# Optimization experiments

Hardware: AMD Instinct MI355X
Metric: run time of the kernel (lower is better)

## Reference

```python
import jax, jax.numpy as jnp
import numpy as np

# irreps: input = 32x0e + 16x1o (dim 80); key/query/value = 8x0e + 4x1o (dim 20); lmax = 1
N_NODES = 10000
N_EDGES = 160000
MUL0_IN, MUL1_IN = 32, 16
MUL0_OUT, MUL1_OUT = 8, 4
NUM_BASIS = 32
HIDDEN = 32
MAX_RADIUS = 2.5
NUM_NEIGHBORS = 32
# per-edge fully-connected TP weight blocks (paths: 0e*0e->0e, 1o*1o->0e, 0e*1o->1o, 1o*0e->1o)
S00 = MUL0_IN * MUL0_OUT    # 256
S110 = MUL1_IN * MUL0_OUT   # 128
S01 = MUL0_IN * MUL1_OUT    # 128
S10 = MUL1_IN * MUL1_OUT    # 64
WNUMEL = S00 + S110 + S01 + S10  # 576
SQRT3 = 1.7320508075688772


def _split_irreps(z, mul0, mul1):
    return z[:, :mul0], z[:, mul0:].reshape(-1, mul1, 3)


def _basis_net(rb, w1, w2):
    # e3nn FullyConnectedNet([num_basis, 32, weight_numel], silu): x @ W / sqrt(fan_in)
    h = jax.nn.silu(rb @ w1 / jnp.sqrt(float(NUM_BASIS)))
    return h @ w2 / jnp.sqrt(float(HIDDEN))


def _edge_tp(x0, x1, Y1, w):
    # FullyConnectedTensorProduct with per-edge weights w [E, WNUMEL].
    # e3nn component/element normalization: path_weight = sqrt(dim(ir_out)/fan_in),
    # fan_in per output irrep = MUL0_IN + MUL1_IN = 48; CG(1,1,0)=CG(0,1,1)=delta/sqrt(3).
    c = 1.0 / jnp.sqrt(float(MUL0_IN + MUL1_IN))
    w00 = w[:, :S00].reshape(-1, MUL0_IN, MUL0_OUT)
    w110 = w[:, S00:S00 + S110].reshape(-1, MUL1_IN, MUL0_OUT)
    w01 = w[:, S00 + S110:S00 + S110 + S01].reshape(-1, MUL0_IN, MUL1_OUT)
    w10 = w[:, S00 + S110 + S01:].reshape(-1, MUL1_IN, MUL1_OUT)
    x1dotY = jnp.einsum('eum,em->eu', x1, Y1)  # [E, MUL1_IN]
    out0 = c * (jnp.einsum('euw,eu->ew', w00, x0)
                + jnp.einsum('euw,eu->ew', w110, x1dotY) / SQRT3)
    out1 = c * (jnp.einsum('euw,eu->ew', w01, x0)[:, :, None] * Y1[:, None, :]
                + jnp.einsum('euw,eum->ewm', w10, x1))
    return out0, out1  # [E, MUL0_OUT], [E, MUL1_OUT, 3]


def _forward(x, pos, w_q0, w_q1, w_kb1, w_kb2, w_vb1, w_vb2, w_sim0, w_sim1, edge_index):
    src, dst = edge_index[0], edge_index[1]
    vec = pos[src] - pos[dst]                                   # [E,3]
    r = jnp.sqrt(jnp.sum(vec * vec, axis=1) + 1e-24)            # [E]
    # bessel soft_one_hot_linspace (cutoff=True), scaled by sqrt(num_basis)
    n = jnp.arange(1, NUM_BASIS + 1, dtype=jnp.float32)
    rb = jnp.sqrt(2.0 / MAX_RADIUS) * jnp.sin(n * jnp.pi * r[:, None] / MAX_RADIUS) / r[:, None]
    rb = rb * jnp.sqrt(float(NUM_BASIS))
    # soft_unit_step(10*(1 - r/max_radius)) = exp(-1/t) for t > 0 else 0
    t = 10.0 * (1.0 - r / MAX_RADIUS)
    cutoff = jnp.where(t > 0.0, jnp.exp(-1.0 / jnp.maximum(t, 1e-12)), 0.0)
    # spherical harmonics lmax=1, 'component' norm: Y0 = 1, Y1 = sqrt(3)*unit_vec
    Y1 = SQRT3 * vec / r[:, None]
    x0, x1 = _split_irreps(x, MUL0_IN, MUL1_IN)
    # o3.Linear query projection: independent per-l blocks, / sqrt(fan_in)
    q0 = x0 @ w_q0 / jnp.sqrt(float(MUL0_IN))                   # [N,8]
    q1 = jnp.einsum('num,uw->nwm', x1, w_q1) / jnp.sqrt(float(MUL1_IN))  # [N,4,3]
    wk = _basis_net(rb, w_kb1, w_kb2)                           # [E,576]
    wv = _basis_net(rb, w_vb1, w_vb2)                           # [E,576]
    x0s, x1s = x0[src], x1[src]
    k0, k1 = _edge_tp(x0s, x1s, Y1, wk)
    v0, v1 = _edge_tp(x0s, x1s, Y1, wv)
    # similarity TP (query x key -> 0e): fan_in = 8*8 + 4*4 = 80
    cs = 1.0 / jnp.sqrt(float(MUL0_OUT ** 2 + MUL1_OUT ** 2))
    sim = cs * (jnp.einsum('uv,eu,ev->e', w_sim0, q0[src], k0)
                + jnp.einsum('uv,eum,evm->e', w_sim1, q1[src], k1) / SQRT3)
    logits = cutoff * sim
    # segment softmax grouped by src node
    m = jax.ops.segment_max(logits, src, num_segments=N_NODES)
    m = jnp.where(jnp.isfinite(m), m, 0.0)
    ex = jnp.exp(logits - m[src])
    den = jax.ops.segment_sum(ex, src, num_segments=N_NODES)
    attn = ex / den[src]                                        # [E]
    a = jnp.sqrt(jax.nn.relu(attn))[:, None]                    # [E,1]
    vals = jnp.concatenate([v0, v1.reshape(-1, MUL1_OUT * 3)], axis=1)  # [E,20]
    return jax.ops.segment_sum(a * vals, dst, num_segments=N_NODES) / NUM_NEIGHBORS


def setup_inputs():
    key = jax.random.key(0)
    ks = jax.random.split(key, 11)
    return {
        'x': jax.random.normal(ks[0], (N_NODES, MUL0_IN + 3 * MUL1_IN), jnp.float32),
        'pos': jax.random.uniform(ks[1], (N_NODES, 3), jnp.float32) * MAX_RADIUS,
        'w_q0': jax.random.normal(ks[2], (MUL0_IN, MUL0_OUT), jnp.float32),
        'w_q1': jax.random.normal(ks[3], (MUL1_IN, MUL1_OUT), jnp.float32),
        'w_kb1': jax.random.normal(ks[4], (NUM_BASIS, HIDDEN), jnp.float32),
        'w_kb2': jax.random.normal(ks[5], (HIDDEN, WNUMEL), jnp.float32),
        'w_vb1': jax.random.normal(ks[6], (NUM_BASIS, HIDDEN), jnp.float32),
        'w_vb2': jax.random.normal(ks[7], (HIDDEN, WNUMEL), jnp.float32),
        'w_sim0': jax.random.normal(ks[8], (MUL0_OUT, MUL0_OUT), jnp.float32),
        'w_sim1': jax.random.normal(ks[9], (MUL1_OUT, MUL1_OUT), jnp.float32),
        'edge_index': jax.random.randint(ks[10], (2, N_EDGES), 0, N_NODES, dtype=jnp.int32),
    }


def reference(x, pos, w_q0, w_q1, w_kb1, w_kb2, w_vb1, w_vb2, w_sim0, w_sim1, edge_index):
    return _forward(x, pos, w_q0, w_q1, w_kb1, w_kb2, w_vb1, w_vb2, w_sim0, w_sim1, edge_index)
```

## Files before the change

kernel.cpp:

```cpp
#include <hip/hip_runtime.h>
#include <hip/hip_fp16.h>
#include <math.h>

#define NN 10000
#define NE 160000

typedef _Float16 half8 __attribute__((ext_vector_type(8)));
typedef __attribute__((ext_vector_type(4))) float f32x4;

constexpr float SQRT3f    = 1.7320508075688772f;
constexpr float ISQRT3    = 0.57735026918962576f;
constexpr float ISQRT32   = 0.17677669529663687f;
constexpr float C_TP      = 0.14433756729740645f;
constexpr float CSIM      = 0.11180339887498949f;
constexpr float PREB      = 5.0596442562694074f;
constexpr float PI_OVER_R = 1.2566370614359172f;
constexpr float INV_RMAX  = 0.4f;
constexpr float HKSC      = C_TP * ISQRT32;
constexpr float DEN_SCALE = 16777216.0f;
constexpr float DEN_INV   = 1.0f / 16777216.0f;
constexpr float OUT_SCALE = 8388608.0f;
constexpr float OUT_INV   = 1.0f / 8388608.0f;

__device__ __forceinline__ unsigned fkey(float f) {
  unsigned u = __float_as_uint(f);
  return (u & 0x80000000u) ? ~u : (u | 0x80000000u);
}
__device__ __forceinline__ float funkey(unsigned k) {
  return (k & 0x80000000u) ? __uint_as_float(k ^ 0x80000000u)
                           : __uint_as_float(~k);
}
__device__ __forceinline__ unsigned short f2h(float f) {
  return __half_as_ushort(__float2half(f));
}

__device__ __forceinline__ int origcol(int n) {
  if (n >= 576) return 512 + (n - 576);
  int w = n / 48, u = n % 48;
  if (w < 8) return (u < 32) ? (u * 8 + w) : (256 + (u - 32) * 8 + w);
  return (u < 32) ? (384 + u * 4 + (w - 8)) : -1;
}

__global__ void __launch_bounds__(256) k_prep(
    const float* __restrict__ w_vb1, const float* __restrict__ w_vb2,
    const float* __restrict__ w_kb1,
    float* __restrict__ W1vt, float* __restrict__ W1kt,
    unsigned short* __restrict__ Wtv)
{
  int tid = blockIdx.x * 256 + threadIdx.x;
  if (tid < 640 * 32) {
    int n = tid >> 5, h = tid & 31;
    int oc = origcol(n);
    float v = (oc >= 0) ? w_vb2[h * 576 + oc] : 0.0f;
    Wtv[n * 32 + h] = f2h(v);
  }
  if (tid < 1024) {
    int h = tid >> 5, n2 = tid & 31;
    W1vt[h * 32 + n2] = w_vb1[n2 * 32 + h];
  } else if (tid < 2048) {
    int j = tid - 1024;
    int h = j >> 5, n2 = j & 31;
    W1kt[h * 32 + n2] = w_kb1[n2 * 32 + h];
  }
}

__global__ void __launch_bounds__(256) k_node(
    const float* __restrict__ x, const float* __restrict__ w_q0,
    const float* __restrict__ w_q1, const float* __restrict__ w_sim0,
    const float* __restrict__ w_sim1,
    float* __restrict__ qs0, float* __restrict__ qs1)
{
  int n = blockIdx.x * 256 + threadIdx.x;
  if (n >= NN) return;
  float x0[32], x1f[48];
  const float4* xr = (const float4*)(x + 80 * n);
#pragma unroll
  for (int i = 0; i < 8; ++i) {
    float4 v = xr[i];
    x0[4*i]=v.x; x0[4*i+1]=v.y; x0[4*i+2]=v.z; x0[4*i+3]=v.w;
  }
#pragma unroll
  for (int i = 0; i < 12; ++i) {
    float4 v = xr[8 + i];
    x1f[4*i]=v.x; x1f[4*i+1]=v.y; x1f[4*i+2]=v.z; x1f[4*i+3]=v.w;
  }
  float q0[8];
#pragma unroll
  for (int w = 0; w < 8; ++w) {
    float a = 0.f;
#pragma unroll
    for (int u = 0; u < 32; ++u) a = fmaf(x0[u], w_q0[u * 8 + w], a);
    q0[w] = a * ISQRT32;
  }
  float q1[12];
#pragma unroll
  for (int w = 0; w < 4; ++w)
#pragma unroll
    for (int m = 0; m < 3; ++m) {
      float a = 0.f;
#pragma unroll
      for (int u = 0; u < 16; ++u) a = fmaf(x1f[3*u+m], w_q1[u*4+w], a);
      q1[w * 3 + m] = a * 0.25f;
    }
#pragma unroll
  for (int v = 0; v < 8; ++v) {
    float a = 0.f;
#pragma unroll
    for (int u = 0; u < 8; ++u) a = fmaf(w_sim0[u * 8 + v], q0[u], a);
    qs0[n * 8 + v] = CSIM * a;
  }
#pragma unroll
  for (int v = 0; v < 4; ++v)
#pragma unroll
    for (int m = 0; m < 3; ++m) {
      float a = 0.f;
#pragma unroll
      for (int u = 0; u < 4; ++u) a = fmaf(w_sim1[u*4+v], q1[u*3+m], a);
      qs1[n * 12 + v * 3 + m] = (CSIM * ISQRT3) * a;
    }
}

template <int HALF>
__global__ void __launch_bounds__(256) k_nodeF(
    const float* __restrict__ x, const float* __restrict__ w_kb2,
    const float* __restrict__ qs0g, const float* __restrict__ qs1g,
    float* __restrict__ nodeF)
{
  __shared__ float W2f[16 * 577];
  __shared__ float ndl[16][100];

  const int tid = threadIdx.x;
  const int nb = blockIdx.x * 16;

#pragma unroll
  for (int i = 0; i < 36; ++i) {
    int idx = i * 256 + tid;
    int row = idx / 576, col = idx - row * 576;
    W2f[row * 577 + col] = w_kb2[(HALF * 16 + row) * 576 + col];
  }
  for (int j = tid; j < 1600; j += 256) {
    int nn = j / 100, jj = j - nn * 100;
    int n = nb + nn;
    float v;
    if (jj < 80)      v = x[80 * n + jj];
    else if (jj < 88) v = qs0g[8 * n + (jj - 80)];
    else              v = qs1g[12 * n + (jj - 88)];
    ndl[nn][jj] = v;
  }
  __syncthreads();

  const int nn = tid >> 4, hh = tid & 15;
  const float* Wh = W2f + hh * 577;
  const float* nd = ndl[nn];

  float t14 = 0.f;
#pragma unroll
  for (int a = 0; a < 32; ++a) {
    float tmp = 0.f;
#pragma unroll
    for (int v = 0; v < 8; ++v) tmp = fmaf(Wh[a * 8 + v], nd[80 + v], tmp);
    t14 = fmaf(tmp, nd[a], t14);
  }
#pragma unroll
  for (int a = 0; a < 16; ++a)
#pragma unroll
    for (int v = 0; v < 4; ++v) {
      float dotv = fmaf(nd[32 + 3*a], nd[88 + 3*v],
                   fmaf(nd[32 + 3*a + 1], nd[88 + 3*v + 1],
                        nd[32 + 3*a + 2] * nd[88 + 3*v + 2]));
      t14 = fmaf(Wh[512 + a * 4 + v], dotv, t14);
    }

  float F0 = 0.f, F1 = 0.f, F2 = 0.f;
#pragma unroll
  for (int a = 0; a < 16; ++a) {
    float q = 0.f;
#pragma unroll
    for (int v = 0; v < 8; ++v) q = fmaf(Wh[256 + a * 8 + v], nd[80 + v], q);
    F0 = fmaf(q, nd[32 + 3*a],     F0);
    F1 = fmaf(q, nd[32 + 3*a + 1], F1);
    F2 = fmaf(q, nd[32 + 3*a + 2], F2);
  }
  F0 *= ISQRT3; F1 *= ISQRT3; F2 *= ISQRT3;
#pragma unroll
  for (int v = 0; v < 4; ++v) {
    float rr = 0.f;
#pragma unroll
    for (int a = 0; a < 32; ++a) rr = fmaf(Wh[384 + a * 4 + v], nd[a], rr);
    F0 = fmaf(rr, nd[88 + 3*v],     F0);
    F1 = fmaf(rr, nd[88 + 3*v + 1], F1);
    F2 = fmaf(rr, nd[88 + 3*v + 2], F2);
  }

  const int n = nb + nn, h = HALF * 16 + hh;
  *(float4*)(nodeF + (size_t)(n * 32 + h) * 4) = make_float4(t14, F0, F1, F2);
}

__global__ void __launch_bounds__(256) k_edgelogit(
    const float* __restrict__ pos,
    const int* __restrict__ esrc, const int* __restrict__ edst,
    const float* __restrict__ W1vt, const float* __restrict__ W1kt,
    const float* __restrict__ nodeF,
    unsigned* __restrict__ hv2, float* __restrict__ geom,
    float* __restrict__ logits, unsigned* __restrict__ mkey)
{
  int e = blockIdx.x * 256 + threadIdx.x;
  if (e >= NE) return;
  int s = esrc[e], d = edst[e];
  float vx = pos[3*s]   - pos[3*d];
  float vy = pos[3*s+1] - pos[3*d+1];
  float vz = pos[3*s+2] - pos[3*d+2];
  float r = sqrtf(fmaf(vx, vx, fmaf(vy, vy, vz * vz)) + 1e-24f);
  float inv_r = 1.0f / r;

  float rb[32];
  {
    float sn, cth;
    sincosf(PI_OVER_R * r, &sn, &cth);
    float twoc = 2.0f * cth, pre = PREB * inv_r, snm1 = 0.0f;
#pragma unroll
    for (int n = 0; n < 32; ++n) {
      rb[n] = pre * sn;
      float t = fmaf(twoc, sn, -snm1);
      snm1 = sn; sn = t;
    }
  }
  float Yx = SQRT3f * vx * inv_r, Yy = SQRT3f * vy * inv_r, Yz = SQRT3f * vz * inv_r;
  float tc = 10.0f * (1.0f - r * INV_RMAX);
  float cut = (tc > 0.0f) ? __expf(-1.0f / tc) : 0.0f;
  *(float4*)(geom + 4 * e) = make_float4(Yx, Yy, Yz, cut);

  const float4* nf = (const float4*)(nodeF) + (size_t)s * 32;
  float sim = 0.f;
#pragma unroll 1
  for (int h2 = 0; h2 < 16; ++h2) {
    const float* wv0 = W1vt + (2 * h2) * 32;
    const float* wv1 = wv0 + 32;
    const float* wk0 = W1kt + (2 * h2) * 32;
    const float* wk1 = wk0 + 32;
    float av0 = 0.f, av1 = 0.f, ak0 = 0.f, ak1 = 0.f;
#pragma unroll
    for (int n = 0; n < 32; ++n) {
      float rn = rb[n];
      av0 = fmaf(rn, wv0[n], av0);
      av1 = fmaf(rn, wv1[n], av1);
      ak0 = fmaf(rn, wk0[n], ak0);
      ak1 = fmaf(rn, wk1[n], ak1);
    }
    av0 *= ISQRT32; av1 *= ISQRT32; ak0 *= ISQRT32; ak1 *= ISQRT32;
    float hv0 = av0 / (1.0f + __expf(-av0)) * HKSC;
    float hv1 = av1 / (1.0f + __expf(-av1)) * HKSC;
    hv2[(size_t)h2 * NE + e] = (unsigned)f2h(hv0) | ((unsigned)f2h(hv1) << 16);
    float hk0 = ak0 / (1.0f + __expf(-ak0)) * HKSC;
    float hk1 = ak1 / (1.0f + __expf(-ak1)) * HKSC;
    float4 f0 = nf[2 * h2], f1 = nf[2 * h2 + 1];
    float S0 = fmaf(f0.y, Yx, fmaf(f0.z, Yy, fmaf(f0.w, Yz, f0.x)));
    float S1 = fmaf(f1.y, Yx, fmaf(f1.z, Yy, fmaf(f1.w, Yz, f1.x)));
    sim = fmaf(hk0, S0, fmaf(hk1, S1, sim));
  }
  float lg = cut * sim;
  logits[e] = lg;
  atomicMax(mkey + s, fkey(lg));
}

__global__ void __launch_bounds__(256) k_den(
    const float* __restrict__ logits, const int* __restrict__ esrc,
    const unsigned* __restrict__ mkey,
    float* __restrict__ exb, int* __restrict__ deni)
{
  int e = blockIdx.x * 256 + threadIdx.x;
  if (e >= NE) return;
  int s = esrc[e];
  float m = funkey(mkey[s]);
  float ex = expf(logits[e] - m);
  exb[e] = ex;
  atomicAdd(&deni[s], __float2int_rn(ex * DEN_SCALE));
}

__global__ void __launch_bounds__(256) k_tpv(
    const unsigned* __restrict__ hv2, const unsigned short* __restrict__ Wtv,
    const float* __restrict__ x, const float* __restrict__ geom,
    const int* __restrict__ esrc, const int* __restrict__ edst,
    const float* __restrict__ exb, const int* __restrict__ deni,
    int* __restrict__ outi)
{
  __shared__ __align__(16) unsigned short Bls[18432];
  __shared__ __align__(16) _Float16 g_lds[4][16 * 52];
  __shared__ __align__(16) _Float16 x1_lds[4][16 * 52];

  const int l = threadIdx.x & 63, wv = threadIdx.x >> 6;
  const int G = l >> 4, c = l & 15;
  const int ebase = (blockIdx.x * 4 + wv) * 16;

  {
    const uint4* src = (const uint4*)Wtv;
    uint4* dst4 = (uint4*)Bls;
#pragma unroll
    for (int i = 0; i < 9; ++i)
      dst4[i * 256 + threadIdx.x] = src[i * 256 + threadIdx.x];
  }
  union H4 { _Float16 h[4]; unsigned long long u; };
#pragma unroll
  for (int i = 0; i < 5; ++i) {
    int idx = i * 64 + l;
    int ee = idx / 20, q = idx - 20 * ee;
    int ss = esrc[ebase + ee];
    float4 v = *(const float4*)(x + 80 * ss + 4 * q);
    H4 p; p.h[0] = (_Float16)v.x; p.h[1] = (_Float16)v.y;
    p.h[2] = (_Float16)v.z; p.h[3] = (_Float16)v.w;
    if (q < 8)
      *(unsigned long long*)(&g_lds[wv][ee * 52 + 4 * q]) = p.u;
    else
      *(unsigned long long*)(&x1_lds[wv][ee * 52 + 4 * q - 32]) = p.u;
  }
  {
    int ee = l >> 2, ug = l & 3;
    int ss = esrc[ebase + ee];
    float4 gm = *(const float4*)(geom + 4 * (ebase + ee));
    const float* xp = x + 80 * ss + 32 + 12 * ug;
    float4 p0 = *(const float4*)(xp);
    float4 p1 = *(const float4*)(xp + 4);
    float4 p2 = *(const float4*)(xp + 8);
    H4 o;
    o.h[0] = (_Float16)(ISQRT3 * fmaf(p0.x, gm.x, fmaf(p0.y, gm.y, p0.z * gm.z)));
    o.h[1] = (_Float16)(ISQRT3 * fmaf(p0.w, gm.x, fmaf(p1.x, gm.y, p1.y * gm.z)));
    o.h[2] = (_Float16)(ISQRT3 * fmaf(p1.z, gm.x, fmaf(p1.w, gm.y, p2.x * gm.z)));
    o.h[3] = (_Float16)(ISQRT3 * fmaf(p2.y, gm.x, fmaf(p2.z, gm.y, p2.w * gm.z)));
    *(unsigned long long*)(&g_lds[wv][ee * 52 + 32 + 4 * ug]) = o.u;
  }
  union { unsigned u[4]; half8 h8; } ua;
#pragma unroll
  for (int j = 0; j < 4; ++j)
    ua.u[j] = hv2[(size_t)(4 * G + j) * NE + ebase + c];
  half8 a8 = ua.h8;

  __syncthreads();

  half8 bt[4];
#pragma unroll
  for (int t = 0; t < 4; ++t)
    bt[t] = *(const half8*)(Wtv + ((36 + t) * 16 + c) * 32 + 8 * G);

  float gh[4][3];
#pragma unroll
  for (int r = 0; r < 4; ++r)
#pragma unroll
    for (int j = 0; j < 3; ++j)
      gh[r][j] = (float)g_lds[wv][(4 * G + r) * 52 + 16 * j + c];

  float vacc[4][12];
#pragma unroll
  for (int r = 0; r < 4; ++r)
#pragma unroll
    for (int w = 0; w < 12; ++w) vacc[r][w] = 0.0f;
  float ot1[4][3];
#pragma unroll
  for (int r = 0; r < 4; ++r) { ot1[r][0]=0.f; ot1[r][1]=0.f; ot1[r][2]=0.f; }

  const f32x4 zero4 = {0.f, 0.f, 0.f, 0.f};
#pragma unroll
  for (int t = 0; t < 36; ++t) {
    union { uint4 u; half8 h; } cvt;
    cvt.u = *(const uint4*)(Bls + (t * 16 + c) * 32 + 8 * G);
    f32x4 dd = __builtin_amdgcn_mfma_f32_16x16x32_f16(a8, cvt.h, zero4, 0, 0, 0);
    const int w = t / 3, j = t % 3;
#pragma unroll
    for (int r = 0; r < 4; ++r)
      vacc[r][w] = fmaf(dd[r], gh[r][j], vacc[r][w]);
  }
#pragma unroll
  for (int t = 0; t < 4; ++t) {
    f32x4 dd = __builtin_amdgcn_mfma_f32_16x16x32_f16(a8, bt[t], zero4, 0, 0, 0);
    const int u = 4 * t + (c >> 2);
#pragma unroll
    for (int r = 0; r < 4; ++r) {
      const _Float16* xp = &x1_lds[wv][(4 * G + r) * 52 + 3 * u];
      ot1[r][0] = fmaf(dd[r], (float)xp[0], ot1[r][0]);
      ot1[r][1] = fmaf(dd[r], (float)xp[1], ot1[r][1]);
      ot1[r][2] = fmaf(dd[r], (float)xp[2], ot1[r][2]);
    }
  }

#pragma unroll
  for (int m = 1; m < 16; m <<= 1)
#pragma unroll
    for (int r = 0; r < 4; ++r)
#pragma unroll
      for (int w = 0; w < 12; ++w)
        vacc[r][w] += __shfl_xor(vacc[r][w], m);
#pragma unroll
  for (int m = 4; m < 16; m <<= 1)
#pragma unroll
    for (int r = 0; r < 4; ++r)
#pragma unroll
      for (int k = 0; k < 3; ++k)
        ot1[r][k] += __shfl_xor(ot1[r][k], m);

  float treg[4] = {0.f, 0.f, 0.f, 0.f};
#pragma unroll
  for (int w = 0; w < 12; ++w)
    if (c == w) {
#pragma unroll
      for (int r = 0; r < 4; ++r) treg[r] = vacc[r][w];
    }

  int sr[4], dst[4]; float4 g4[4]; float a_[4];
#pragma unroll
  for (int r = 0; r < 4; ++r) {
    int eg = ebase + 4 * G + r;
    sr[r] = esrc[eg];
    dst[r] = edst[eg];
    g4[r] = *(const float4*)(geom + 4 * eg);
    float denf = (float)deni[sr[r]] * DEN_INV;
    a_[r] = sqrtf(fmaxf(exb[eg] / denf, 0.f)) * 0.03125f;
  }
  float s01w[4];
#pragma unroll
  for (int r = 0; r < 4; ++r) s01w[r] = __shfl_xor(treg[r], 8);
  if (c < 8) {
#pragma unroll
    for (int r = 0; r < 4; ++r)
      atomicAdd(outi + 20 * dst[r] + c,
                __float2int_rn(a_[r] * treg[r] * OUT_SCALE));
  }
  if (c < 4) {
#pragma unroll
    for (int r = 0; r < 4; ++r) {
      float vx_ = fmaf(s01w[r], g4[r].x, ot1[r][0]);
      float vy_ = fmaf(s01w[r], g4[r].y, ot1[r][1]);
      float vz_ = fmaf(s01w[r], g4[r].z, ot1[r][2]);
      atomicAdd(outi + 20 * dst[r] + 8 + 3 * c + 0,
                __float2int_rn(a_[r] * vx_ * OUT_SCALE));
      atomicAdd(outi + 20 * dst[r] + 8 + 3 * c + 1,
                __float2int_rn(a_[r] * vy_ * OUT_SCALE));
      atomicAdd(outi + 20 * dst[r] + 8 + 3 * c + 2,
                __float2int_rn(a_[r] * vz_ * OUT_SCALE));
    }
  }
}

__global__ void __launch_bounds__(256) k_out(
    const int* __restrict__ outi, float* __restrict__ out)
{
  int i = blockIdx.x * 256 + threadIdx.x;
  if (i < NN * 20) out[i] = (float)outi[i] * OUT_INV;
}

extern "C" void kernel_launch(void* const* d_in, const int* in_sizes, int n_in,
                              void* d_out, int out_size, void* d_ws, size_t ws_size,
                              hipStream_t stream)
{
  const float* x      = (const float*)d_in[0];
  const float* pos    = (const float*)d_in[1];
  const float* w_q0   = (const float*)d_in[2];
  const float* w_q1   = (const float*)d_in[3];
  const float* w_kb1  = (const float*)d_in[4];
  const float* w_kb2  = (const float*)d_in[5];
  const float* w_vb1  = (const float*)d_in[6];
  const float* w_vb2  = (const float*)d_in[7];
  const float* w_sim0 = (const float*)d_in[8];
  const float* w_sim1 = (const float*)d_in[9];
  const int*   eidx   = (const int*)d_in[10];
  const int* esrc = eidx;
  const int* edst = eidx + NE;
  float* out = (float*)d_out;

  float* ws      = (float*)d_ws;
  float* geom    = ws;
  float* qs0     = geom + (size_t)NE * 4;
  float* qs1     = qs0 + NN * 8;
  float* logits  = qs1 + NN * 12;
  float* exb     = logits + NE;
  float* nodeF   = exb + NE;
  float* W1vt    = nodeF + (size_t)NN * 128;
  float* W1kt    = W1vt + 1024;
  int*   deni    = (int*)(W1kt + 1024);
  unsigned* mkey = (unsigned*)(deni + NN);
  int*   outi    = (int*)(mkey + NN);
  unsigned* hv2  = (unsigned*)(outi + NN * 20);
  unsigned short* Wtv = (unsigned short*)(hv2 + (size_t)16 * NE);

  hipMemsetAsync(deni, 0, (size_t)(NN * 22) * sizeof(int), stream);

  const int eb = (NE + 255) / 256;
  k_prep<<<dim3(80), dim3(256), 0, stream>>>(
      w_vb1, w_vb2, w_kb1, W1vt, W1kt, Wtv);
  k_node<<<dim3((NN + 255) / 256), dim3(256), 0, stream>>>(
      x, w_q0, w_q1, w_sim0, w_sim1, qs0, qs1);
  k_nodeF<0><<<dim3(NN / 16), dim3(256), 0, stream>>>(
      x, w_kb2, qs0, qs1, nodeF);
  k_nodeF<1><<<dim3(NN / 16), dim3(256), 0, stream>>>(
      x, w_kb2, qs0, qs1, nodeF);
  k_edgelogit<<<dim3(eb), dim3(256), 0, stream>>>(
      pos, esrc, edst, W1vt, W1kt, nodeF, hv2, geom, logits, mkey);
  k_den<<<dim3(eb), dim3(256), 0, stream>>>(logits, esrc, mkey, exb, deni);
  k_tpv<<<dim3(NE / 64), dim3(256), 0, stream>>>(
      hv2, Wtv, x, geom, esrc, edst, exb, deni, outi);
  k_out<<<dim3((NN * 20 + 255) / 256), dim3(256), 0, stream>>>(outi, out);
}
```

Measured before the change: 199.5 us.

## Merge prep/node kernels and nodeF halves; keep TP-V gathers in fp32 LDS

Merges the weight-prep and node-projection kernels into one launch split by block index, and merges the two nodeF template instantiations into a single 1250-block launch. This cuts two kernel launches and their serialization gaps. In k_tpv, gathered source features and geometry dot products now stay in fp32 LDS instead of being packed to fp16. The gh register cache is dropped, so g_lds is read inside the MFMA loop, which adds LDS traffic and doubles the LDS footprint of those buffers.

```diff
diff --git a/kernel.cpp b/kernel.cpp
--- a/kernel.cpp
+++ b/kernel.cpp
@@ -41,36 +41,35 @@
   return (u < 32) ? (384 + u * 4 + (w - 8)) : -1;
 }
 
-__global__ void __launch_bounds__(256) k_prep(
+__global__ void __launch_bounds__(256) k_setup(
     const float* __restrict__ w_vb1, const float* __restrict__ w_vb2,
     const float* __restrict__ w_kb1,
-    float* __restrict__ W1vt, float* __restrict__ W1kt,
-    unsigned short* __restrict__ Wtv)
-{
-  int tid = blockIdx.x * 256 + threadIdx.x;
-  if (tid < 640 * 32) {
-    int n = tid >> 5, h = tid & 31;
-    int oc = origcol(n);
-    float v = (oc >= 0) ? w_vb2[h * 576 + oc] : 0.0f;
-    Wtv[n * 32 + h] = f2h(v);
-  }
-  if (tid < 1024) {
-    int h = tid >> 5, n2 = tid & 31;
-    W1vt[h * 32 + n2] = w_vb1[n2 * 32 + h];
-  } else if (tid < 2048) {
-    int j = tid - 1024;
-    int h = j >> 5, n2 = j & 31;
-    W1kt[h * 32 + n2] = w_kb1[n2 * 32 + h];
-  }
-}
-
-__global__ void __launch_bounds__(256) k_node(
     const float* __restrict__ x, const float* __restrict__ w_q0,
     const float* __restrict__ w_q1, const float* __restrict__ w_sim0,
     const float* __restrict__ w_sim1,
+    float* __restrict__ W1vt, float* __restrict__ W1kt,
+    unsigned short* __restrict__ Wtv,
     float* __restrict__ qs0, float* __restrict__ qs1)
 {
-  int n = blockIdx.x * 256 + threadIdx.x;
+  if (blockIdx.x < 80) {
+    int tid = blockIdx.x * 256 + threadIdx.x;
+    if (tid < 640 * 32) {
+      int n = tid >> 5, h = tid & 31;
+      int oc = origcol(n);
+      float v = (oc >= 0) ? w_vb2[h * 576 + oc] : 0.0f;
+      Wtv[n * 32 + h] = f2h(v);
+    }
+    if (tid < 1024) {
+      int h = tid >> 5, n2 = tid & 31;
+      W1vt[h * 32 + n2] = w_vb1[n2 * 32 + h];
+    } else if (tid < 2048) {
+      int j = tid - 1024;
+      int h = j >> 5, n2 = j & 31;
+      W1kt[h * 32 + n2] = w_kb1[n2 * 32 + h];
+    }
+    return;
+  }
+  int n = (blockIdx.x - 80) * 256 + threadIdx.x;
   if (n >= NN) return;
   float x0[32], x1f[48];
   const float4* xr = (const float4*)(x + 80 * n);
@@ -120,7 +119,6 @@
     }
 }
 
-template <int HALF>
 __global__ void __launch_bounds__(256) k_nodeF(
     const float* __restrict__ x, const float* __restrict__ w_kb2,
     const float* __restrict__ qs0g, const float* __restrict__ qs1g,
@@ -130,7 +128,8 @@
   __shared__ float ndl[16][100];
 
   const int tid = threadIdx.x;
-  const int nb = blockIdx.x * 16;
+  const int HALF = (blockIdx.x >= 625) ? 1 : 0;
+  const int nb = (blockIdx.x - HALF * 625) * 16;
 
 #pragma unroll
   for (int i = 0; i < 36; ++i) {
@@ -284,35 +283,34 @@
     const float* __restrict__ exb, const int* __restrict__ deni,
     int* __restrict__ outi)
 {
-  __shared__ __align__(16) unsigned short Bls[18432];
-  __shared__ __align__(16) _Float16 g_lds[4][16 * 52];
-  __shared__ __align__(16) _Float16 x1_lds[4][16 * 52];
+  __shared__ __align__(16) uint4  wlds4[2304];
+  __shared__ __align__(16) float g_lds[4][16 * 52];
+  __shared__ __align__(16) float x1_lds[4][16 * 52];
 
   const int l = threadIdx.x & 63, wv = threadIdx.x >> 6;
+  const int tile = blockIdx.x * 4 + wv;
   const int G = l >> 4, c = l & 15;
-  const int ebase = (blockIdx.x * 4 + wv) * 16;
-
-  {
-    const uint4* src = (const uint4*)Wtv;
-    uint4* dst4 = (uint4*)Bls;
-#pragma unroll
-    for (int i = 0; i < 9; ++i)
-      dst4[i * 256 + threadIdx.x] = src[i * 256 + threadIdx.x];
-  }
-  union H4 { _Float16 h[4]; unsigned long long u; };
+  const int ebase = tile * 16;
+
+  const uint4* Wt4 = (const uint4*)Wtv;
+#pragma unroll
+  for (int i = 0; i < 9; ++i) {
+    int chunk = i * 256 + threadIdx.x;
+    wlds4[chunk] = Wt4[chunk];
+  }
+
 #pragma unroll
   for (int i = 0; i < 5; ++i) {
     int idx = i * 64 + l;
     int ee = idx / 20, q = idx - 20 * ee;
     int ss = esrc[ebase + ee];
     float4 v = *(const float4*)(x + 80 * ss + 4 * q);
-    H4 p; p.h[0] = (_Float16)v.x; p.h[1] = (_Float16)v.y;
-    p.h[2] = (_Float16)v.z; p.h[3] = (_Float16)v.w;
     if (q < 8)
-      *(unsigned long long*)(&g_lds[wv][ee * 52 + 4 * q]) = p.u;
+      *(float4*)(&g_lds[wv][ee * 52 + 4 * q]) = v;
     else
-      *(unsigned long long*)(&x1_lds[wv][ee * 52 + 4 * q - 32]) = p.u;
-  }
+      *(float4*)(&x1_lds[wv][ee * 52 + 4 * q - 32]) = v;
+  }
+
   {
     int ee = l >> 2, ug = l & 3;
     int ss = esrc[ebase + ee];
@@ -321,13 +319,14 @@
     float4 p0 = *(const float4*)(xp);
     float4 p1 = *(const float4*)(xp + 4);
     float4 p2 = *(const float4*)(xp + 8);
-    H4 o;
-    o.h[0] = (_Float16)(ISQRT3 * fmaf(p0.x, gm.x, fmaf(p0.y, gm.y, p0.z * gm.z)));
-    o.h[1] = (_Float16)(ISQRT3 * fmaf(p0.w, gm.x, fmaf(p1.x, gm.y, p1.y * gm.z)));
-    o.h[2] = (_Float16)(ISQRT3 * fmaf(p1.z, gm.x, fmaf(p1.w, gm.y, p2.x * gm.z)));
-    o.h[3] = (_Float16)(ISQRT3 * fmaf(p2.y, gm.x, fmaf(p2.z, gm.y, p2.w * gm.z)));
-    *(unsigned long long*)(&g_lds[wv][ee * 52 + 32 + 4 * ug]) = o.u;
-  }
+    float4 o;
+    o.x = ISQRT3 * fmaf(p0.x, gm.x, fmaf(p0.y, gm.y, p0.z * gm.z));
+    o.y = ISQRT3 * fmaf(p0.w, gm.x, fmaf(p1.x, gm.y, p1.y * gm.z));
+    o.z = ISQRT3 * fmaf(p1.z, gm.x, fmaf(p1.w, gm.y, p2.x * gm.z));
+    o.w = ISQRT3 * fmaf(p2.y, gm.x, fmaf(p2.z, gm.y, p2.w * gm.z));
+    *(float4*)(&g_lds[wv][ee * 52 + 32 + 4 * ug]) = o;
+  }
+
   union { unsigned u[4]; half8 h8; } ua;
 #pragma unroll
   for (int j = 0; j < 4; ++j)
@@ -341,13 +340,6 @@
   for (int t = 0; t < 4; ++t)
     bt[t] = *(const half8*)(Wtv + ((36 + t) * 16 + c) * 32 + 8 * G);
 
-  float gh[4][3];
-#pragma unroll
-  for (int r = 0; r < 4; ++r)
-#pragma unroll
-    for (int j = 0; j < 3; ++j)
-      gh[r][j] = (float)g_lds[wv][(4 * G + r) * 52 + 16 * j + c];
-
   float vacc[4][12];
 #pragma unroll
   for (int r = 0; r < 4; ++r)
@@ -361,12 +353,12 @@
 #pragma unroll
   for (int t = 0; t < 36; ++t) {
     union { uint4 u; half8 h; } cvt;
-    cvt.u = *(const uint4*)(Bls + (t * 16 + c) * 32 + 8 * G);
+    cvt.u = wlds4[(t * 16 + c) * 4 + G];
     f32x4 dd = __builtin_amdgcn_mfma_f32_16x16x32_f16(a8, cvt.h, zero4, 0, 0, 0);
-    const int w = t / 3, j = t % 3;
+    const int w = t / 3, u0 = (t % 3) * 16;
 #pragma unroll
     for (int r = 0; r < 4; ++r)
-      vacc[r][w] = fmaf(dd[r], gh[r][j], vacc[r][w]);
+      vacc[r][w] = fmaf(dd[r], g_lds[wv][(4 * G + r) * 52 + u0 + c], vacc[r][w]);
   }
 #pragma unroll
   for (int t = 0; t < 4; ++t) {
@@ -374,10 +366,10 @@
     const int u = 4 * t + (c >> 2);
 #pragma unroll
     for (int r = 0; r < 4; ++r) {
-      const _Float16* xp = &x1_lds[wv][(4 * G + r) * 52 + 3 * u];
-      ot1[r][0] = fmaf(dd[r], (float)xp[0], ot1[r][0]);
-      ot1[r][1] = fmaf(dd[r], (float)xp[1], ot1[r][1]);
-      ot1[r][2] = fmaf(dd[r], (float)xp[2], ot1[r][2]);
+      const float* xp = &x1_lds[wv][(4 * G + r) * 52 + 3 * u];
+      ot1[r][0] = fmaf(dd[r], xp[0], ot1[r][0]);
+      ot1[r][1] = fmaf(dd[r], xp[1], ot1[r][1]);
+      ot1[r][2] = fmaf(dd[r], xp[2], ot1[r][2]);
     }
   }
 
@@ -483,13 +475,10 @@
   hipMemsetAsync(deni, 0, (size_t)(NN * 22) * sizeof(int), stream);
 
   const int eb = (NE + 255) / 256;
-  k_prep<<<dim3(80), dim3(256), 0, stream>>>(
-      w_vb1, w_vb2, w_kb1, W1vt, W1kt, Wtv);
-  k_node<<<dim3((NN + 255) / 256), dim3(256), 0, stream>>>(
-      x, w_q0, w_q1, w_sim0, w_sim1, qs0, qs1);
-  k_nodeF<0><<<dim3(NN / 16), dim3(256), 0, stream>>>(
-      x, w_kb2, qs0, qs1, nodeF);
-  k_nodeF<1><<<dim3(NN / 16), dim3(256), 0, stream>>>(
+  k_setup<<<dim3(120), dim3(256), 0, stream>>>(
+      w_vb1, w_vb2, w_kb1, x, w_q0, w_q1, w_sim0, w_sim1,
+      W1vt, W1kt, Wtv, qs0, qs1);
+  k_nodeF<<<dim3(1250), dim3(256), 0, stream>>>(
       x, w_kb2, qs0, qs1, nodeF);
   k_edgelogit<<<dim3(eb), dim3(256), 0, stream>>>(
       pos, esrc, edst, W1vt, W1kt, nodeF, hv2, geom, logits, mkey);
```

After: 190.7 us. 4.4% less time.
